# Optimization experiments

Measured on AMD Instinct MI355X. Metric: run time of the kernel, lower is better.

## Reference

```python
import jax, jax.numpy as jnp
import numpy as np

N_NODES = 50000
N_EDGES = 600000
D = 128
HIDDEN = 128
OUT = 1


def setup_inputs() -> dict:
    key = jax.random.key(0)
    ks = jax.random.split(key, 6)
    z = jax.random.normal(ks[0], (N_NODES, D), dtype=jnp.float32)
    e = jax.random.randint(ks[1], (2, N_EDGES), 0, N_NODES, dtype=jnp.int64)
    # Linear weights in [in, out] layout; scaled like torch default init
    W1 = jax.random.normal(ks[2], (2 * D, HIDDEN), dtype=jnp.float32) / np.sqrt(2 * D)
    b1 = jax.random.normal(ks[3], (HIDDEN,), dtype=jnp.float32) / np.sqrt(2 * D)
    W2 = jax.random.normal(ks[4], (HIDDEN, OUT), dtype=jnp.float32) / np.sqrt(HIDDEN)
    b2 = jax.random.normal(ks[5], (OUT,), dtype=jnp.float32) / np.sqrt(HIDDEN)
    return {"z": z, "e": e, "W1": W1, "b1": b1, "W2": W2, "b2": b2}


def reference(z, e, W1, b1, W2, b2):
    x_i = z[e[0]]                      # [E, D] gather source nodes
    x_j = z[e[1]]                      # [E, D] gather target nodes
    x = jnp.concatenate([x_i, x_j], axis=1)  # [E, 2D]
    h = jax.nn.relu(x @ W1 + b1)       # [E, HIDDEN]
    out = h @ W2 + b2                  # [E, OUT]
    return jax.nn.sigmoid(out).squeeze()  # [E]
```

## Files before the change

### kernel.cpp

```cpp
#include <hip/hip_runtime.h>


#define DD 128

typedef __attribute__((ext_vector_type(8))) short short8;
typedef __attribute__((ext_vector_type(4))) float floatx4;

static __device__ __forceinline__ unsigned short f2bf(float f) {
  unsigned int u = __builtin_bit_cast(unsigned int, f);
  u += 0x7fffu + ((u >> 16) & 1u);
  return (unsigned short)(u >> 16);
}
static __device__ __forceinline__ float bflo(unsigned int u) {
  return __builtin_bit_cast(float, u << 16);
}
static __device__ __forceinline__ float bfhi(unsigned int u) {
  return __builtin_bit_cast(float, u & 0xffff0000u);
}

__global__ __launch_bounds__(256) void wt_build(
    const float* __restrict__ W1, unsigned short* __restrict__ Wt) {
  const int g = blockIdx.x * 256 + threadIdx.x;
  const int c = g >> 5;
  const int kq = (g & 31) * 4;
  const float* src = (c < 128) ? (W1 + c) : (W1 + 128 * 128 + (c - 128));
  ushort4 o;
  o.x = f2bf(src[(size_t)(kq + 0) * 128]);
  o.y = f2bf(src[(size_t)(kq + 1) * 128]);
  o.z = f2bf(src[(size_t)(kq + 2) * 128]);
  o.w = f2bf(src[(size_t)(kq + 3) * 128]);
  *(ushort4*)&Wt[c * 128 + kq] = o;
}

__global__ __launch_bounds__(256) void node_mfma(
    const float* __restrict__ z, const unsigned short* __restrict__ Wt,
    const float* __restrict__ b1, unsigned short* __restrict__ gi,
    unsigned short* __restrict__ gj, int n_nodes) {
  __shared__ unsigned short zb[64 * 136];
  const int tid = threadIdx.x;
  const int nb = blockIdx.x * 64;

#pragma unroll
  for (int i = 0; i < 8; ++i) {
    int q = tid + i * 256;
    int nl = q >> 5;
    int node = nb + nl; if (node >= n_nodes) node = n_nodes - 1;
    float4 v = ((const float4*)z)[(size_t)node * 32 + (q & 31)];
    ushort4 o;
    o.x = f2bf(v.x); o.y = f2bf(v.y); o.z = f2bf(v.z); o.w = f2bf(v.w);
    *(ushort4*)&zb[nl * 136 + (q & 31) * 4] = o;
  }

  const int w = tid >> 6, lane = tid & 63;
  const int l15 = lane & 15, quad = lane >> 4;

  short8 a[4][4];
#pragma unroll
  for (int tt = 0; tt < 4; ++tt) {
    const unsigned short* wrow =
        Wt + (size_t)((w * 4 + tt) * 16 + l15) * 128 + quad * 8;
#pragma unroll
    for (int s = 0; s < 4; ++s) a[tt][s] = *(const short8*)(wrow + s * 32);
  }

  floatx4 acc[4][4];
#pragma unroll
  for (int tt = 0; tt < 4; ++tt) {
    floatx4 bias = {0.f, 0.f, 0.f, 0.f};
    if (w < 2) {
      float4 b4 = *(const float4*)&b1[(w * 4 + tt) * 16 + quad * 4];
      bias[0] = b4.x; bias[1] = b4.y; bias[2] = b4.z; bias[3] = b4.w;
    }
#pragma unroll
    for (int nt = 0; nt < 4; ++nt) acc[tt][nt] = bias;
  }

  __syncthreads();

#pragma unroll
  for (int nt = 0; nt < 4; ++nt) {
    short8 bz[4];
#pragma unroll
    for (int s = 0; s < 4; ++s)
      bz[s] = *(const short8*)&zb[(nt * 16 + l15) * 136 + s * 32 + quad * 8];
#pragma unroll
    for (int tt = 0; tt < 4; ++tt)
#pragma unroll
      for (int s = 0; s < 4; ++s)
        acc[tt][nt] =
            __builtin_amdgcn_mfma_f32_16x16x32_bf16(a[tt][s], bz[s], acc[tt][nt], 0, 0, 0);
  }

  unsigned short* base = (w < 2) ? gi : gj;
  const int cbase = w * 64 - ((w < 2) ? 0 : 128);
#pragma unroll
  for (int nt = 0; nt < 4; ++nt) {
    const int node = nb + nt * 16 + l15;
    if (node < n_nodes) {
#pragma unroll
      for (int tt = 0; tt < 4; ++tt) {
        const int c = cbase + tt * 16 + quad * 4;
        ushort4 o;
        o.x = f2bf(acc[tt][nt][0]); o.y = f2bf(acc[tt][nt][1]);
        o.z = f2bf(acc[tt][nt][2]); o.w = f2bf(acc[tt][nt][3]);
        *(ushort4*)&base[(size_t)node * 128 + c] = o;
      }
    }
  }
}

static __device__ __forceinline__ float dot8(uint4 a, uint4 b, float4 w0, float4 w1) {
  float s;
  s = fmaxf(bflo(a.x) + bflo(b.x), 0.f) * w0.x;
  s = fmaf(fmaxf(bfhi(a.x) + bfhi(b.x), 0.f), w0.y, s);
  s = fmaf(fmaxf(bflo(a.y) + bflo(b.y), 0.f), w0.z, s);
  s = fmaf(fmaxf(bfhi(a.y) + bfhi(b.y), 0.f), w0.w, s);
  s = fmaf(fmaxf(bflo(a.z) + bflo(b.z), 0.f), w1.x, s);
  s = fmaf(fmaxf(bfhi(a.z) + bfhi(b.z), 0.f), w1.y, s);
  s = fmaf(fmaxf(bflo(a.w) + bflo(b.w), 0.f), w1.z, s);
  s = fmaf(fmaxf(bfhi(a.w) + bfhi(b.w), 0.f), w1.w, s);
  return s;
}

__global__ __launch_bounds__(256) void edge_mlp(
    const int* __restrict__ e, const unsigned short* __restrict__ gi,
    const unsigned short* __restrict__ gj, const float* __restrict__ W2,
    const float* __restrict__ b2, float* __restrict__ out, int E) {
  const int p = threadIdx.x & 7;
  const float4* wv = (const float4*)W2;
  const float4 w0 = wv[p * 2],      w1 = wv[p * 2 + 1];
  const float4 w2 = wv[16 + p * 2], w3 = wv[16 + p * 2 + 1];
  const float bias2 = b2[0];

  const int stride = gridDim.x * 32;
  for (int edge = blockIdx.x * 32 + (threadIdx.x >> 3); edge < E; edge += stride) {
    const int i = e[edge];
    const int j = e[E + edge];
    const uint4* pi = (const uint4*)(gi + (size_t)i * 128);
    const uint4* pj = (const uint4*)(gj + (size_t)j * 128);
    uint4 a0 = pi[p], a1 = pi[8 + p];
    uint4 c0 = pj[p], c1 = pj[8 + p];
    float acc = dot8(a0, c0, w0, w1) + dot8(a1, c1, w2, w3);
    acc += __shfl_xor(acc, 1);
    acc += __shfl_xor(acc, 2);
    acc += __shfl_xor(acc, 4);
    if (p == 0) {
      float x = acc + bias2;
      out[edge] = 1.f / (1.f + __expf(-x));
    }
  }
}

__global__ __launch_bounds__(256) void edge_direct(
    const int* __restrict__ e, const float* __restrict__ z,
    const float* __restrict__ W1, const float* __restrict__ b1,
    const float* __restrict__ W2, const float* __restrict__ b2,
    float* __restrict__ out, int E) {
  const int lane = threadIdx.x & 63;
  const int edge = (int)((blockIdx.x * 256u + threadIdx.x) >> 6);
  if (edge >= E) return;
  const int i = e[edge], j = e[E + edge];
  const float* zi = z + (size_t)i * 128;
  const float* zj = z + (size_t)j * 128;
  const int c0 = lane * 2;
  float h0 = b1[c0], h1 = b1[c0 + 1];
  for (int k = 0; k < 128; ++k) {
    float a = zi[k], b = zj[k];
    float2 wt = *(const float2*)&W1[(size_t)k * 128 + c0];
    float2 wb = *(const float2*)&W1[(size_t)(128 + k) * 128 + c0];
    h0 = fmaf(a, wt.x, h0); h1 = fmaf(a, wt.y, h1);
    h0 = fmaf(b, wb.x, h0); h1 = fmaf(b, wb.y, h1);
  }
  float s = fmaxf(h0, 0.f) * W2[c0] + fmaxf(h1, 0.f) * W2[c0 + 1];
#pragma unroll
  for (int off = 1; off < 64; off <<= 1) s += __shfl_xor(s, off);
  if (lane == 0) out[edge] = 1.f / (1.f + __expf(-(s + b2[0])));
}

extern "C" void kernel_launch(void* const* d_in, const int* in_sizes, int n_in,
                              void* d_out, int out_size, void* d_ws, size_t ws_size,
                              hipStream_t stream) {
  const float* z  = (const float*)d_in[0];
  const int*   e  = (const int*)d_in[1];
  const float* W1 = (const float*)d_in[2];
  const float* b1 = (const float*)d_in[3];
  const float* W2 = (const float*)d_in[4];
  const float* b2 = (const float*)d_in[5];
  float* out = (float*)d_out;
  const int n_nodes = in_sizes[0] / DD;
  const int E = in_sizes[1] / 2;

  const size_t g_bytes = (size_t)n_nodes * DD * sizeof(unsigned short);
  const size_t wt_bytes = 256 * 128 * sizeof(unsigned short);
  if (ws_size >= 2 * g_bytes + wt_bytes) {
    unsigned short* gi = (unsigned short*)d_ws;
    unsigned short* gj = (unsigned short*)((char*)d_ws + g_bytes);
    unsigned short* Wt = (unsigned short*)((char*)d_ws + 2 * g_bytes);
    wt_build<<<32, 256, 0, stream>>>(W1, Wt);
    node_mfma<<<(n_nodes + 63) / 64, 256, 0, stream>>>(z, Wt, b1, gi, gj, n_nodes);
    edge_mlp<<<2048, 256, 0, stream>>>(e, gi, gj, W2, b2, out, E);
  } else {
    edge_direct<<<(E + 3) / 4, 256, 0, stream>>>(e, z, W1, b1, W2, b2, out, E);
  }
}
```

Before: 134.3 us.

## Counting-sort edges by source node before gathered edge MLP

After: 202.7 us. +50.9%, slower.

```diff
diff --git a/kernel.cpp b/kernel.cpp
--- a/kernel.cpp
+++ b/kernel.cpp
@@ -2,6 +2,8 @@
 
 
 #define DD 128
+#define NBINS 50176
+#define SORT_BLOCKS 196
 
 typedef __attribute__((ext_vector_type(8))) short short8;
 typedef __attribute__((ext_vector_type(4))) float floatx4;
@@ -109,6 +111,73 @@
   }
 }
 
+__global__ __launch_bounds__(256) void k_zero(int* __restrict__ counts) {
+  counts[blockIdx.x * 256 + threadIdx.x] = 0;
+}
+
+__global__ __launch_bounds__(256) void k_hist(
+    const int* __restrict__ e, int* __restrict__ counts, int E) {
+  int t = blockIdx.x * 256 + threadIdx.x;
+  if (t < E) atomicAdd(&counts[e[t]], 1);
+}
+
+__global__ __launch_bounds__(256) void k_scan1(
+    const int* __restrict__ counts, int* __restrict__ pref,
+    int* __restrict__ bsum) {
+  __shared__ int s[256];
+  const int t = threadIdx.x;
+  const int g = blockIdx.x * 256 + t;
+  int v = counts[g];
+  s[t] = v;
+  __syncthreads();
+#pragma unroll
+  for (int off = 1; off < 256; off <<= 1) {
+    int x = 0;
+    if (t >= off) x = s[t - off];
+    __syncthreads();
+    if (t >= off) s[t] += x;
+    __syncthreads();
+  }
+  pref[g] = s[t] - v;
+  if (t == 255) bsum[blockIdx.x] = s[255];
+}
+
+__global__ __launch_bounds__(256) void k_scan2(
+    const int* __restrict__ bsum, int* __restrict__ boff) {
+  __shared__ int s[256];
+  const int t = threadIdx.x;
+  int v = (t < SORT_BLOCKS) ? bsum[t] : 0;
+  s[t] = v;
+  __syncthreads();
+#pragma unroll
+  for (int off = 1; off < 256; off <<= 1) {
+    int x = 0;
+    if (t >= off) x = s[t - off];
+    __syncthreads();
+    if (t >= off) s[t] += x;
+    __syncthreads();
+  }
+  if (t < SORT_BLOCKS) boff[t] = s[t] - v;
+}
+
+__global__ __launch_bounds__(256) void k_cursor(
+    const int* __restrict__ pref, const int* __restrict__ boff,
+    int* __restrict__ cursor) {
+  const int g = blockIdx.x * 256 + threadIdx.x;
+  cursor[g] = pref[g] + boff[g >> 8];
+}
+
+__global__ __launch_bounds__(256) void k_scatter(
+    const int* __restrict__ e, int* __restrict__ cursor,
+    int4* __restrict__ sorted, int E) {
+  int t = blockIdx.x * 256 + threadIdx.x;
+  if (t < E) {
+    int i = e[t], j = e[E + t];
+    int pos = atomicAdd(&cursor[i], 1);
+    sorted[pos] = make_int4(i, j, t, 0);
+  }
+}
+
 static __device__ __forceinline__ float dot8(uint4 a, uint4 b, float4 w0, float4 w1) {
   float s;
   s = fmaxf(bflo(a.x) + bflo(b.x), 0.f) * w0.x;
@@ -122,22 +191,22 @@
   return s;
 }
 
-__global__ __launch_bounds__(256) void edge_mlp(
-    const int* __restrict__ e, const unsigned short* __restrict__ gi,
+__global__ __launch_bounds__(256) void edge_mlp_sorted(
+    const int4* __restrict__ sorted, const unsigned short* __restrict__ gi,
     const unsigned short* __restrict__ gj, const float* __restrict__ W2,
-    const float* __restrict__ b2, float* __restrict__ out, int E) {
+    const float* __restrict__ b2, float* __restrict__ out, int E, int chunk) {
   const int p = threadIdx.x & 7;
   const float4* wv = (const float4*)W2;
   const float4 w0 = wv[p * 2],      w1 = wv[p * 2 + 1];
   const float4 w2 = wv[16 + p * 2], w3 = wv[16 + p * 2 + 1];
   const float bias2 = b2[0];
 
-  const int stride = gridDim.x * 32;
-  for (int edge = blockIdx.x * 32 + (threadIdx.x >> 3); edge < E; edge += stride) {
-    const int i = e[edge];
-    const int j = e[E + edge];
-    const uint4* pi = (const uint4*)(gi + (size_t)i * 128);
-    const uint4* pj = (const uint4*)(gj + (size_t)j * 128);
+  const int start = blockIdx.x * chunk;
+  const int end   = min(start + chunk, E);
+  for (int k = start + (threadIdx.x >> 3); k < end; k += 32) {
+    const int4 s = sorted[k];
+    const uint4* pi = (const uint4*)(gi + (size_t)s.x * 128);
+    const uint4* pj = (const uint4*)(gj + (size_t)s.y * 128);
     uint4 a0 = pi[p], a1 = pi[8 + p];
     uint4 c0 = pj[p], c1 = pj[8 + p];
     float acc = dot8(a0, c0, w0, w1) + dot8(a1, c1, w2, w3);
@@ -146,7 +215,7 @@
     acc += __shfl_xor(acc, 4);
     if (p == 0) {
       float x = acc + bias2;
-      out[edge] = 1.f / (1.f + __expf(-x));
+      out[s.z] = 1.f / (1.f + __expf(-x));
     }
   }
 }
@@ -190,15 +259,37 @@
   const int n_nodes = in_sizes[0] / DD;
   const int E = in_sizes[1] / 2;
 
-  const size_t g_bytes = (size_t)n_nodes * DD * sizeof(unsigned short);
+  const size_t g_bytes  = (size_t)n_nodes * DD * sizeof(unsigned short);
   const size_t wt_bytes = 256 * 128 * sizeof(unsigned short);
-  if (ws_size >= 2 * g_bytes + wt_bytes) {
-    unsigned short* gi = (unsigned short*)d_ws;
-    unsigned short* gj = (unsigned short*)((char*)d_ws + g_bytes);
-    unsigned short* Wt = (unsigned short*)((char*)d_ws + 2 * g_bytes);
+  const size_t sort_bytes = (size_t)E * sizeof(int4);
+  const size_t bin_bytes  = (size_t)NBINS * sizeof(int);
+  const size_t need = 2 * g_bytes + wt_bytes + sort_bytes + 3 * bin_bytes +
+                      2 * 256 * sizeof(int) + 256;
+
+  if (ws_size >= need && n_nodes <= NBINS) {
+    char* p = (char*)d_ws;
+    unsigned short* gi = (unsigned short*)p;        p += g_bytes;
+    unsigned short* gj = (unsigned short*)p;        p += g_bytes;
+    unsigned short* Wt = (unsigned short*)p;        p += wt_bytes;
+    int4* sorted       = (int4*)p;                  p += sort_bytes;
+    int* counts        = (int*)p;                   p += bin_bytes;
+    int* pref          = (int*)p;                   p += bin_bytes;
+    int* cursor        = (int*)p;                   p += bin_bytes;
+    int* bsum          = (int*)p;                   p += 256 * sizeof(int);
+    int* boff          = (int*)p;
+
     wt_build<<<32, 256, 0, stream>>>(W1, Wt);
+    k_zero<<<SORT_BLOCKS, 256, 0, stream>>>(counts);
     node_mfma<<<(n_nodes + 63) / 64, 256, 0, stream>>>(z, Wt, b1, gi, gj, n_nodes);
-    edge_mlp<<<2048, 256, 0, stream>>>(e, gi, gj, W2, b2, out, E);
+    k_hist<<<(E + 255) / 256, 256, 0, stream>>>(e, counts, E);
+    k_scan1<<<SORT_BLOCKS, 256, 0, stream>>>(counts, pref, bsum);
+    k_scan2<<<1, 256, 0, stream>>>(bsum, boff);
+    k_cursor<<<SORT_BLOCKS, 256, 0, stream>>>(pref, boff, cursor);
+    k_scatter<<<(E + 255) / 256, 256, 0, stream>>>(e, cursor, sorted, E);
+
+    const int nblk = 2048;
+    const int chunk = (E + nblk - 1) / nblk;
+    edge_mlp_sorted<<<nblk, 256, 0, stream>>>(sorted, gi, gj, W2, b2, out, E, chunk);
   } else {
     edge_direct<<<(E + 3) / 4, 256, 0, stream>>>(e, z, W1, b1, W2, b2, out, E);
   }
```

## Bucket-sort edges by source node block before edge MLP gather

Applied to the files above, without the earlier changes.

Result: slower. 160.7 us (+19.6%).

```diff
diff --git a/kernel.cpp b/kernel.cpp
--- a/kernel.cpp
+++ b/kernel.cpp
@@ -2,6 +2,8 @@
 
 
 #define DD 128
+#define NCHUNK 128
+#define NBMAX 1024
 
 typedef __attribute__((ext_vector_type(8))) short short8;
 typedef __attribute__((ext_vector_type(4))) float floatx4;
@@ -109,6 +111,78 @@
   }
 }
 
+__global__ __launch_bounds__(256) void ehist(
+    const int* __restrict__ e, int* __restrict__ counts, int E, int NB, int chunk) {
+  __shared__ int h[NBMAX];
+  const int c = blockIdx.x;
+  for (int b = threadIdx.x; b < NB; b += 256) h[b] = 0;
+  __syncthreads();
+  const int start = c * chunk, end = min(start + chunk, E);
+  for (int t = start + threadIdx.x; t < end; t += 256)
+    atomicAdd(&h[((unsigned)e[t]) >> 6], 1);
+  __syncthreads();
+  for (int b = threadIdx.x; b < NB; b += 256)
+    counts[b * NCHUNK + c] = h[b];
+}
+
+__global__ __launch_bounds__(256) void scanA(
+    const int* __restrict__ counts, int* __restrict__ part,
+    int* __restrict__ bsum, int M) {
+  __shared__ int s[256];
+  const int t = threadIdx.x;
+  const int g = blockIdx.x * 256 + t;
+  int v = (g < M) ? counts[g] : 0;
+  s[t] = v;
+  __syncthreads();
+#pragma unroll
+  for (int off = 1; off < 256; off <<= 1) {
+    int x = 0;
+    if (t >= off) x = s[t - off];
+    __syncthreads();
+    if (t >= off) s[t] += x;
+    __syncthreads();
+  }
+  if (g < M) part[g] = s[t] - v;
+  if (t == 255) bsum[blockIdx.x] = s[255];
+}
+
+__global__ __launch_bounds__(512) void scanB(int* __restrict__ bsum, int nA) {
+  __shared__ int s[512];
+  const int t = threadIdx.x;
+  int v = (t < nA) ? bsum[t] : 0;
+  s[t] = v;
+  __syncthreads();
+#pragma unroll
+  for (int off = 1; off < 512; off <<= 1) {
+    int x = 0;
+    if (t >= off) x = s[t - off];
+    __syncthreads();
+    if (t >= off) s[t] += x;
+    __syncthreads();
+  }
+  if (t < nA) bsum[t] = s[t] - v;
+}
+
+__global__ __launch_bounds__(256) void escatter(
+    const int* __restrict__ e, const int* __restrict__ part,
+    const int* __restrict__ bsum, uint2* __restrict__ sorted,
+    int E, int NB, int chunk) {
+  __shared__ int cur[NBMAX];
+  const int c = blockIdx.x;
+  for (int b = threadIdx.x; b < NB; b += 256) {
+    const int idx = b * NCHUNK + c;
+    cur[b] = part[idx] + bsum[idx >> 8];
+  }
+  __syncthreads();
+  const int start = c * chunk, end = min(start + chunk, E);
+  for (int t = start + threadIdx.x; t < end; t += 256) {
+    const unsigned i = (unsigned)e[t];
+    const unsigned j = (unsigned)e[E + t];
+    const int pos = atomicAdd(&cur[i >> 6], 1);
+    sorted[pos] = make_uint2((j << 16) | i, (unsigned)t);
+  }
+}
+
 static __device__ __forceinline__ float dot8(uint4 a, uint4 b, float4 w0, float4 w1) {
   float s;
   s = fmaxf(bflo(a.x) + bflo(b.x), 0.f) * w0.x;
@@ -122,6 +196,37 @@
   return s;
 }
 
+__global__ __launch_bounds__(256) void edge_sorted(
+    const uint2* __restrict__ sorted, const unsigned short* __restrict__ gi,
+    const unsigned short* __restrict__ gj, const float* __restrict__ W2,
+    const float* __restrict__ b2, float* __restrict__ out, int E, int chunk) {
+  const int p = threadIdx.x & 7;
+  const float4* wv = (const float4*)W2;
+  const float4 w0 = wv[p * 2],      w1 = wv[p * 2 + 1];
+  const float4 w2 = wv[16 + p * 2], w3 = wv[16 + p * 2 + 1];
+  const float bias2 = b2[0];
+
+  const int start = blockIdx.x * chunk;
+  const int end = min(start + chunk, E);
+  for (int k = start + (threadIdx.x >> 3); k < end; k += 32) {
+    const uint2 s = sorted[k];
+    const int i = s.x & 0xffff;
+    const int j = s.x >> 16;
+    const uint4* pi = (const uint4*)(gi + (size_t)i * 128);
+    const uint4* pj = (const uint4*)(gj + (size_t)j * 128);
+    uint4 a0 = pi[p], a1 = pi[8 + p];
+    uint4 c0 = pj[p], c1 = pj[8 + p];
+    float acc = dot8(a0, c0, w0, w1) + dot8(a1, c1, w2, w3);
+    acc += __shfl_xor(acc, 1);
+    acc += __shfl_xor(acc, 2);
+    acc += __shfl_xor(acc, 4);
+    if (p == 0) {
+      float x = acc + bias2;
+      out[s.y] = 1.f / (1.f + __expf(-x));
+    }
+  }
+}
+
 __global__ __launch_bounds__(256) void edge_mlp(
     const int* __restrict__ e, const unsigned short* __restrict__ gi,
     const unsigned short* __restrict__ gj, const float* __restrict__ W2,
@@ -131,7 +236,6 @@
   const float4 w0 = wv[p * 2],      w1 = wv[p * 2 + 1];
   const float4 w2 = wv[16 + p * 2], w3 = wv[16 + p * 2 + 1];
   const float bias2 = b2[0];
-
   const int stride = gridDim.x * 32;
   for (int edge = blockIdx.x * 32 + (threadIdx.x >> 3); edge < E; edge += stride) {
     const int i = e[edge];
@@ -190,15 +294,43 @@
   const int n_nodes = in_sizes[0] / DD;
   const int E = in_sizes[1] / 2;
 
-  const size_t g_bytes = (size_t)n_nodes * DD * sizeof(unsigned short);
+  const size_t g_bytes  = (size_t)n_nodes * DD * sizeof(unsigned short);
   const size_t wt_bytes = 256 * 128 * sizeof(unsigned short);
-  if (ws_size >= 2 * g_bytes + wt_bytes) {
-    unsigned short* gi = (unsigned short*)d_ws;
-    unsigned short* gj = (unsigned short*)((char*)d_ws + g_bytes);
-    unsigned short* Wt = (unsigned short*)((char*)d_ws + 2 * g_bytes);
+  const int NB = (n_nodes + 63) >> 6;
+  const int M  = NB * NCHUNK;
+  const int nA = (M + 255) / 256;
+  const size_t sort_bytes = (size_t)E * sizeof(uint2);
+  const size_t cnt_bytes  = (size_t)M * sizeof(int);
+  const size_t need_base  = 2 * g_bytes + wt_bytes;
+  const size_t need_sort  = need_base + sort_bytes + 2 * cnt_bytes + 512 * sizeof(int);
+
+  if (ws_size >= need_base) {
+    char* p = (char*)d_ws;
+    unsigned short* gi = (unsigned short*)p;  p += g_bytes;
+    unsigned short* gj = (unsigned short*)p;  p += g_bytes;
+    unsigned short* Wt = (unsigned short*)p;  p += wt_bytes;
+
     wt_build<<<32, 256, 0, stream>>>(W1, Wt);
     node_mfma<<<(n_nodes + 63) / 64, 256, 0, stream>>>(z, Wt, b1, gi, gj, n_nodes);
-    edge_mlp<<<2048, 256, 0, stream>>>(e, gi, gj, W2, b2, out, E);
+
+    if (ws_size >= need_sort && n_nodes <= 65536 && nA <= 512) {
+      uint2* sorted = (uint2*)p;  p += sort_bytes;
+      int* counts   = (int*)p;    p += cnt_bytes;
+      int* part     = (int*)p;    p += cnt_bytes;
+      int* bsum     = (int*)p;
+
+      const int chunk = (E + NCHUNK - 1) / NCHUNK;
+      ehist<<<NCHUNK, 256, 0, stream>>>(e, counts, E, NB, chunk);
+      scanA<<<nA, 256, 0, stream>>>(counts, part, bsum, M);
+      scanB<<<1, 512, 0, stream>>>(bsum, nA);
+      escatter<<<NCHUNK, 256, 0, stream>>>(e, part, bsum, sorted, E, NB, chunk);
+
+      const int nblk = 2048;
+      const int echunk = (E + nblk - 1) / nblk;
+      edge_sorted<<<nblk, 256, 0, stream>>>(sorted, gi, gj, W2, b2, out, E, echunk);
+    } else {
+      edge_mlp<<<2048, 256, 0, stream>>>(e, gi, gj, W2, b2, out, E);
+    }
   } else {
     edge_direct<<<(E + 3) / 4, 256, 0, stream>>>(e, z, W1, b1, W2, b2, out, E);
   }
```

## Bucket-sort edges by target node to localize gj gathers, then unpermute outputs

Applied to the files above, without the earlier changes.

Result: slower. 151.8 us (+13.1%).

```diff
diff --git a/kernel.cpp b/kernel.cpp
--- a/kernel.cpp
+++ b/kernel.cpp
@@ -2,9 +2,13 @@
 
 
 #define DD 128
+#define NBUCK 8
+#define PCHUNK 256
+#define BSHIFT 13
 
 typedef __attribute__((ext_vector_type(8))) short short8;
 typedef __attribute__((ext_vector_type(4))) float floatx4;
+typedef __attribute__((ext_vector_type(4))) unsigned int uintx4;
 
 static __device__ __forceinline__ unsigned short f2bf(float f) {
   unsigned int u = __builtin_bit_cast(unsigned int, f);
@@ -109,6 +113,63 @@
   }
 }
 
+__global__ __launch_bounds__(256) void phist(
+    const int* __restrict__ e, int* __restrict__ counts, int E, int chunk) {
+  __shared__ int h[NBUCK];
+  if (threadIdx.x < NBUCK) h[threadIdx.x] = 0;
+  __syncthreads();
+  const int start = blockIdx.x * chunk, end = min(start + chunk, E);
+  for (int t = start + threadIdx.x; t < end; t += 256)
+    atomicAdd(&h[((unsigned)e[E + t]) >> BSHIFT], 1);
+  __syncthreads();
+  if (threadIdx.x < NBUCK)
+    counts[threadIdx.x * PCHUNK + blockIdx.x] = h[threadIdx.x];
+}
+
+__global__ __launch_bounds__(256) void pscan(
+    const int* __restrict__ counts, int* __restrict__ part) {
+  __shared__ int totals[256];
+  const int t = threadIdx.x;
+  int pre[8];
+  int sum = 0;
+#pragma unroll
+  for (int k = 0; k < 8; ++k) {
+    int v = counts[t * 8 + k];
+    pre[k] = sum;
+    sum += v;
+  }
+  totals[t] = sum;
+  __syncthreads();
+#pragma unroll
+  for (int off = 1; off < 256; off <<= 1) {
+    int x = 0;
+    if (t >= off) x = totals[t - off];
+    __syncthreads();
+    if (t >= off) totals[t] += x;
+    __syncthreads();
+  }
+  const int boff = (t == 0) ? 0 : totals[t - 1];
+#pragma unroll
+  for (int k = 0; k < 8; ++k) part[t * 8 + k] = pre[k] + boff;
+}
+
+__global__ __launch_bounds__(256) void pscatter(
+    const int* __restrict__ e, const int* __restrict__ part,
+    uint2* __restrict__ sorted, int* __restrict__ pos, int E, int chunk) {
+  __shared__ int cur[NBUCK];
+  if (threadIdx.x < NBUCK)
+    cur[threadIdx.x] = part[threadIdx.x * PCHUNK + blockIdx.x];
+  __syncthreads();
+  const int start = blockIdx.x * chunk, end = min(start + chunk, E);
+  for (int t = start + threadIdx.x; t < end; t += 256) {
+    const unsigned i = (unsigned)e[t];
+    const unsigned j = (unsigned)e[E + t];
+    const int p = atomicAdd(&cur[j >> BSHIFT], 1);
+    sorted[p] = make_uint2((j << 16) | i, (unsigned)t);
+    pos[t] = p;
+  }
+}
+
 static __device__ __forceinline__ float dot8(uint4 a, uint4 b, float4 w0, float4 w1) {
   float s;
   s = fmaxf(bflo(a.x) + bflo(b.x), 0.f) * w0.x;
@@ -122,6 +183,48 @@
   return s;
 }
 
+static __device__ __forceinline__ uint4 nt_load16(const unsigned int* base) {
+  uintx4 v = __builtin_nontemporal_load((const uintx4*)base);
+  return make_uint4(v.x, v.y, v.z, v.w);
+}
+
+__global__ __launch_bounds__(256) void edge_sweep(
+    const uint2* __restrict__ sorted, const unsigned short* __restrict__ gi,
+    const unsigned short* __restrict__ gj, const float* __restrict__ W2,
+    const float* __restrict__ b2, float* __restrict__ outs, int E) {
+  const int p = threadIdx.x & 7;
+  const float4* wv = (const float4*)W2;
+  const float4 w0 = wv[p * 2],      w1 = wv[p * 2 + 1];
+  const float4 w2 = wv[16 + p * 2], w3 = wv[16 + p * 2 + 1];
+  const float bias2 = b2[0];
+  const int stride = gridDim.x * 32;
+  for (int k = blockIdx.x * 32 + (threadIdx.x >> 3); k < E; k += stride) {
+    const uint2 s = sorted[k];
+    const int i = s.x & 0xffff;
+    const int j = s.x >> 16;
+    const unsigned int* pi = (const unsigned int*)(gi + (size_t)i * 128);
+    const uint4* pj = (const uint4*)(gj + (size_t)j * 128);
+    uint4 a0 = nt_load16(pi + p * 4);
+    uint4 a1 = nt_load16(pi + 32 + p * 4);
+    uint4 c0 = pj[p], c1 = pj[8 + p];
+    float acc = dot8(a0, c0, w0, w1) + dot8(a1, c1, w2, w3);
+    acc += __shfl_xor(acc, 1);
+    acc += __shfl_xor(acc, 2);
+    acc += __shfl_xor(acc, 4);
+    if (p == 0) {
+      float x = acc + bias2;
+      outs[k] = 1.f / (1.f + __expf(-x));
+    }
+  }
+}
+
+__global__ __launch_bounds__(256) void unpermute(
+    const float* __restrict__ outs, const int* __restrict__ pos,
+    float* __restrict__ out, int E) {
+  const int t = blockIdx.x * 256 + threadIdx.x;
+  if (t < E) out[t] = outs[pos[t]];
+}
+
 __global__ __launch_bounds__(256) void edge_mlp(
     const int* __restrict__ e, const unsigned short* __restrict__ gi,
     const unsigned short* __restrict__ gj, const float* __restrict__ W2,
@@ -131,7 +234,6 @@
   const float4 w0 = wv[p * 2],      w1 = wv[p * 2 + 1];
   const float4 w2 = wv[16 + p * 2], w3 = wv[16 + p * 2 + 1];
   const float bias2 = b2[0];
-
   const int stride = gridDim.x * 32;
   for (int edge = blockIdx.x * 32 + (threadIdx.x >> 3); edge < E; edge += stride) {
     const int i = e[edge];
@@ -190,15 +292,41 @@
   const int n_nodes = in_sizes[0] / DD;
   const int E = in_sizes[1] / 2;
 
-  const size_t g_bytes = (size_t)n_nodes * DD * sizeof(unsigned short);
+  const size_t g_bytes  = (size_t)n_nodes * DD * sizeof(unsigned short);
   const size_t wt_bytes = 256 * 128 * sizeof(unsigned short);
-  if (ws_size >= 2 * g_bytes + wt_bytes) {
-    unsigned short* gi = (unsigned short*)d_ws;
-    unsigned short* gj = (unsigned short*)((char*)d_ws + g_bytes);
-    unsigned short* Wt = (unsigned short*)((char*)d_ws + 2 * g_bytes);
+  const size_t sort_bytes = (size_t)E * sizeof(uint2);
+  const size_t pos_bytes  = (size_t)E * sizeof(int);
+  const size_t outs_bytes = (size_t)E * sizeof(float);
+  const size_t cnt_bytes  = (size_t)NBUCK * PCHUNK * sizeof(int);
+  const size_t need_base = 2 * g_bytes + wt_bytes;
+  const size_t need_part =
+      need_base + sort_bytes + pos_bytes + outs_bytes + 2 * cnt_bytes;
+
+  if (ws_size >= need_base) {
+    char* p = (char*)d_ws;
+    unsigned short* gi = (unsigned short*)p;  p += g_bytes;
+    unsigned short* gj = (unsigned short*)p;  p += g_bytes;
+    unsigned short* Wt = (unsigned short*)p;  p += wt_bytes;
+
     wt_build<<<32, 256, 0, stream>>>(W1, Wt);
     node_mfma<<<(n_nodes + 63) / 64, 256, 0, stream>>>(z, Wt, b1, gi, gj, n_nodes);
-    edge_mlp<<<2048, 256, 0, stream>>>(e, gi, gj, W2, b2, out, E);
+
+    if (ws_size >= need_part && n_nodes <= 65536) {
+      uint2* sorted = (uint2*)p;  p += sort_bytes;
+      int* pos      = (int*)p;    p += pos_bytes;
+      float* outs   = (float*)p;  p += outs_bytes;
+      int* counts   = (int*)p;    p += cnt_bytes;
+      int* part     = (int*)p;
+
+      const int chunk = (E + PCHUNK - 1) / PCHUNK;
+      phist<<<PCHUNK, 256, 0, stream>>>(e, counts, E, chunk);
+      pscan<<<1, 256, 0, stream>>>(counts, part);
+      pscatter<<<PCHUNK, 256, 0, stream>>>(e, part, sorted, pos, E, chunk);
+      edge_sweep<<<2048, 256, 0, stream>>>(sorted, gi, gj, W2, b2, outs, E);
+      unpermute<<<(E + 255) / 256, 256, 0, stream>>>(outs, pos, out, E);
+    } else {
+      edge_mlp<<<2048, 256, 0, stream>>>(e, gi, gj, W2, b2, out, E);
+    }
   } else {
     edge_direct<<<(E + 3) / 4, 256, 0, stream>>>(e, z, W1, b1, W2, b2, out, E);
   }
```
